# Kernel tuning notes

Measured on AMD Instinct MI355X. Metric: run time of the kernel, lower is better.

## Reference

```python
import jax, jax.numpy as jnp
import numpy as np
from jax import lax

DILATIONS = (1, 3, 5)
EPS = 1e-5
B, T, C, S, K = 8, 4096, 512, 64, 3


def _adain(x, s, w, b):
    # instance norm over time (axis=1), per (batch, channel), no learned affine;
    # style-conditioned affine: (1+gamma)*xn + beta
    h = s @ w + b                              # (B, 2C)
    gamma, beta = jnp.split(h, 2, axis=-1)     # (B, C) each
    mu = jnp.mean(x, axis=1, keepdims=True)
    var = jnp.var(x, axis=1, keepdims=True)
    xn = (x - mu) * lax.rsqrt(var + EPS)
    return (1.0 + gamma[:, None, :]) * xn + beta[:, None, :]


def _snake(x, alpha):
    # snake activation: x + (1/a) * sin(a*x)^2
    return x + (1.0 / alpha) * jnp.sin(alpha * x) ** 2


def _wn_conv(x, v, g, b, dilation):
    # weight-normalized dilated 1d conv; v: (K, Cin, Cout), norm over (K, Cin)
    norm = jnp.sqrt(jnp.sum(v * v, axis=(0, 1), keepdims=True))
    w = g[None, None, :] * v / norm
    y = lax.conv_general_dilated(x, w, window_strides=(1,), padding='SAME',
                                 rhs_dilation=(dilation,),
                                 dimension_numbers=('NWC', 'WIO', 'NWC'))
    return y + b


def setup_inputs() -> dict:
    key = jax.random.key(0)
    ks = jax.random.split(key, 6)
    return {
        'x': jax.random.normal(ks[0], (B, T, C), dtype=jnp.float32),
        's': jax.random.normal(ks[1], (B, S), dtype=jnp.float32),
        'fc1_w': jax.random.normal(ks[2], (3, S, 2 * C), dtype=jnp.float32) * 0.02,
        'fc1_b': jnp.zeros((3, 2 * C), dtype=jnp.float32),
        'alpha1': jnp.ones((3, 1, 1, C), dtype=jnp.float32),
        'conv1_v': jax.random.normal(ks[3], (3, K, C, C), dtype=jnp.float32),
        'conv1_g': jnp.ones((3, C), dtype=jnp.float32),
        'conv1_b': jnp.zeros((3, C), dtype=jnp.float32),
        'fc2_w': jax.random.normal(ks[4], (3, S, 2 * C), dtype=jnp.float32) * 0.02,
        'fc2_b': jnp.zeros((3, 2 * C), dtype=jnp.float32),
        'alpha2': jnp.ones((3, 1, 1, C), dtype=jnp.float32),
        'conv2_v': jax.random.normal(ks[5], (3, K, C, C), dtype=jnp.float32),
        'conv2_g': jnp.ones((3, C), dtype=jnp.float32),
        'conv2_b': jnp.zeros((3, C), dtype=jnp.float32),
    }


def reference(x, s, fc1_w, fc1_b, alpha1, conv1_v, conv1_g, conv1_b,
              fc2_w, fc2_b, alpha2, conv2_v, conv2_g, conv2_b):
    for i, d in enumerate(DILATIONS):
        xt = _adain(x, s, fc1_w[i], fc1_b[i])
        xt = _snake(xt, alpha1[i])
        xt = _wn_conv(xt, conv1_v[i], conv1_g[i], conv1_b[i], d)
        xt = _adain(xt, s, fc2_w[i], fc2_b[i])
        xt = _snake(xt, alpha2[i])
        xt = _wn_conv(xt, conv2_v[i], conv2_g[i], conv2_b[i], 1)
        x = xt + x
    return x
```

## Files before the change

### kernel.cpp

```cpp
#include <hip/hip_runtime.h>
#include <hip/hip_bf16.h>

#define B_ 8
#define T_ 4096
#define C_ 512
#define S_ 64
#define KT 3
#define EPSC 1e-5f
#define PADB 5
#define RB 4128

typedef __attribute__((ext_vector_type(8))) short bf16x8;
typedef __attribute__((ext_vector_type(4))) float f32x4;
typedef __attribute__((address_space(3))) unsigned int lds_u32_t;
typedef const __attribute__((address_space(1))) unsigned int glb_u32_t;

__device__ inline unsigned short f2bf(float x) {
    __hip_bfloat16 h = __float2bfloat16(x);
    return *reinterpret_cast<unsigned short*>(&h);
}

__global__ void norm_partial(const float* __restrict__ v1, const float* __restrict__ v2,
                             float* __restrict__ normsq) {
    int j = blockIdx.y;
    int i = j >> 1;
    const float* v = ((j & 1) ? v2 : v1) + (size_t)i * KT * C_ * C_;
    int r0 = blockIdx.x * 16;
    int tid = threadIdx.x;
    float a0 = 0.f, a1 = 0.f;
    for (int r = 0; r < 16; ++r) {
        const float* row = v + (size_t)(r0 + r) * C_;
        float x = row[tid];
        float y = row[tid + 256];
        a0 += x * x; a1 += y * y;
    }
    atomicAdd(&normsq[j * C_ + tid], a0);
    atomicAdd(&normsq[j * C_ + tid + 256], a1);
}

__global__ void wt_kernel(const float* __restrict__ v1, const float* __restrict__ v2,
                          const float* __restrict__ g1, const float* __restrict__ g2,
                          const float* __restrict__ normsq, unsigned short* __restrict__ wT) {
    __shared__ float tile[64][65];
    int jk = blockIdx.y;
    int j = jk / 3, k = jk % 3;
    int i = j >> 1;
    const float* v = ((j & 1) ? v2 : v1) + ((size_t)i * KT + k) * C_ * C_;
    const float* g = ((j & 1) ? g2 : g1) + (size_t)i * C_;
    int tci = (blockIdx.x >> 3) * 64;
    int tco = (blockIdx.x & 7) * 64;
    int tid = threadIdx.x;
    int lr = tid >> 6, lc = tid & 63;
    for (int rr = 0; rr < 16; ++rr) {
        int ci = rr * 4 + lr;
        tile[ci][lc] = v[(size_t)(tci + ci) * C_ + tco + lc];
    }
    __syncthreads();
    for (int rr = 0; rr < 16; ++rr) {
        int co_l = rr * 4 + lr;
        int co = tco + co_l;
        float w = g[co] * rsqrtf(normsq[j * C_ + co]) * tile[lc][co_l];
        wT[((size_t)j * KT + k) * C_ * C_ + (size_t)co * C_ + tci + lc] = f2bf(w);
    }
}

__global__ void zero_pads(unsigned short* __restrict__ zp) {
    int q = blockIdx.x * 256 + threadIdx.x;
    int b = q >> 11, r = q & 2047;
    int row = r >> 6;
    int col = (r & 63) * 8;
    int prow = row < PADB ? row : row + T_;
    uint4 zz = make_uint4(0u, 0u, 0u, 0u);
    *(uint4*)(zp + ((size_t)b * RB + prow) * C_ + col) = zz;
}

__global__ void stats_partial(const float* __restrict__ u, float* __restrict__ ssum,
                              float* __restrict__ ssq) {
    int c = blockIdx.y * 256 + threadIdx.x;
    int b = blockIdx.z;
    int t0 = blockIdx.x * 64;
    const float* p = u + ((size_t)b * T_ + t0) * C_ + c;
    float s1 = 0.f, s2 = 0.f;
    for (int t = 0; t < 64; ++t) {
        float x = p[(size_t)t * C_];
        s1 += x; s2 += x * x;
    }
    atomicAdd(&ssum[b * C_ + c], s1);
    atomicAdd(&ssq[b * C_ + c], s2);
}

__global__ void adain_finalize(const float* __restrict__ ssum, const float* __restrict__ ssq,
                               const float* __restrict__ s, const float* __restrict__ fcw,
                               const float* __restrict__ fcb,
                               float* __restrict__ scale, float* __restrict__ shift) {
    int idx = blockIdx.x * 256 + threadIdx.x;
    int b = idx >> 9, c = idx & (C_ - 1);
    float mu = ssum[idx] * (1.f / T_);
    float var = ssq[idx] * (1.f / T_) - mu * mu;
    var = fmaxf(var, 0.f);
    float gamma = fcb[c], beta = fcb[C_ + c];
    const float* sp = s + b * S_;
    for (int p = 0; p < S_; ++p) {
        float sv = sp[p];
        gamma += sv * fcw[p * 2 * C_ + c];
        beta  += sv * fcw[p * 2 * C_ + C_ + c];
    }
    float sc = (1.f + gamma) * rsqrtf(var + EPSC);
    scale[idx] = sc;
    shift[idx] = beta - mu * sc;
}

__global__ void act_kernel(const float* __restrict__ u, const float* __restrict__ scale,
                           const float* __restrict__ shift, const float* __restrict__ alpha,
                           unsigned short* __restrict__ zp) {
    size_t idx4 = (size_t)blockIdx.x * 256 + threadIdx.x;
    size_t e0 = idx4 * 4;
    int c = (int)(e0 & (C_ - 1));
    int b = (int)(e0 >> 21);
    const float4 xv = *(const float4*)(u + e0);
    const float4 scv = *(const float4*)(scale + b * C_ + c);
    const float4 shv = *(const float4*)(shift + b * C_ + c);
    const float4 av = *(const float4*)(alpha + c);
    float xx[4] = {xv.x, xv.y, xv.z, xv.w};
    float ss[4] = {scv.x, scv.y, scv.z, scv.w};
    float hh[4] = {shv.x, shv.y, shv.z, shv.w};
    float aa[4] = {av.x, av.y, av.z, av.w};
    ushort4 o;
    unsigned short r[4];
    #pragma unroll
    for (int q = 0; q < 4; ++q) {
        float val = xx[q] * ss[q] + hh[q];
        float sn = sinf(aa[q] * val);
        r[q] = f2bf(val + sn * sn / aa[q]);
    }
    o.x = r[0]; o.y = r[1]; o.z = r[2]; o.w = r[3];
    size_t dst = ((size_t)b * RB + PADB) * C_ + (e0 & (((size_t)1 << 21) - 1));
    *(ushort4*)(zp + dst) = o;
}

#define BM 128
#define BN 128
#define AR 160

__global__ __launch_bounds__(256) void conv_kernel(
    const unsigned short* __restrict__ zp, const unsigned short* __restrict__ wT,
    const float* __restrict__ bias, const float* __restrict__ residual,
    float* __restrict__ out, float* __restrict__ ssum, float* __restrict__ ssq, int dil) {
    __shared__ unsigned short As[AR * 64];
    __shared__ unsigned short Bs[3 * BN * 64];
    int tid = threadIdx.x;
    int m0 = blockIdx.x * BM;
    int b = m0 >> 12;
    int t0 = m0 & (T_ - 1);
    int n0 = blockIdx.y * BN;
    int wv = tid >> 6;
    int l = tid & 63;
    int wm = (wv >> 1) * 64, wn = (wv & 1) * 64;
    int l16 = l & 15, lg = l >> 4;

    const unsigned short* aBase = zp + ((size_t)b * RB + t0) * C_;
    const unsigned short* bBase = wT + (size_t)n0 * C_;

    f32x4 acc[4][4];
    #pragma unroll
    for (int a = 0; a < 4; ++a)
        #pragma unroll
        for (int q = 0; q < 4; ++q) acc[a][q] = (f32x4){0.f, 0.f, 0.f, 0.f};

    for (int ci0 = 0; ci0 < C_; ci0 += 64) {
        #pragma unroll
        for (int it = 0; it < 5; ++it) {
            int chunk = it * 256 + tid;
            int row = chunk >> 3, c = chunk & 7;
            const unsigned short* src = aBase + (size_t)row * C_ + ci0 + ((c ^ (row & 7)) * 8);
            __builtin_amdgcn_global_load_lds((glb_u32_t*)src,
                (lds_u32_t*)&As[(it * 256 + wv * 64) * 8], 16, 0, 0);
        }
        #pragma unroll
        for (int it = 0; it < 12; ++it) {
            int chunk = it * 256 + tid;
            int row = chunk >> 3, c = chunk & 7;
            int k = row >> 7, co = row & 127;
            const unsigned short* src = bBase + ((size_t)k * C_ + co) * C_ + ci0 + ((c ^ (row & 7)) * 8);
            __builtin_amdgcn_global_load_lds((glb_u32_t*)src,
                (lds_u32_t*)&Bs[(it * 256 + wv * 64) * 8], 16, 0, 0);
        }
        __syncthreads();

        #pragma unroll
        for (int ks = 0; ks < 2; ++ks) {
            #pragma unroll
            for (int k = 0; k < 3; ++k) {
                int sh = (k - 1) * dil + PADB;
                bf16x8 afr[4], bfr[4];
                #pragma unroll
                for (int mf = 0; mf < 4; ++mf) {
                    int row = wm + mf * 16 + l16 + sh;
                    afr[mf] = *(const bf16x8*)(&As[row * 64 + (((ks * 4 + lg) ^ (row & 7)) * 8)]);
                }
                #pragma unroll
                for (int nf = 0; nf < 4; ++nf) {
                    int row = wn + nf * 16 + l16;
                    bfr[nf] = *(const bf16x8*)(&Bs[(k * BN + row) * 64 + (((ks * 4 + lg) ^ (row & 7)) * 8)]);
                }
                #pragma unroll
                for (int mf = 0; mf < 4; ++mf)
                    #pragma unroll
                    for (int nf = 0; nf < 4; ++nf)
                        acc[mf][nf] = __builtin_amdgcn_mfma_f32_16x16x32_bf16(
                            afr[mf], bfr[nf], acc[mf][nf], 0, 0, 0);
            }
        }
        __syncthreads();
    }

    #pragma unroll
    for (int nf = 0; nf < 4; ++nf) {
        int co = n0 + wn + nf * 16 + l16;
        float bv = bias[co];
        float s1 = 0.f, s2 = 0.f;
        #pragma unroll
        for (int mf = 0; mf < 4; ++mf) {
            #pragma unroll
            for (int r = 0; r < 4; ++r) {
                int t = t0 + wm + mf * 16 + lg * 4 + r;
                size_t idx = ((size_t)b * T_ + t) * C_ + co;
                float val = acc[mf][nf][r] + bv;
                if (residual) val += residual[idx];
                out[idx] = val;
                s1 += val; s2 += val * val;
            }
        }
        s1 += __shfl_xor(s1, 16); s1 += __shfl_xor(s1, 32);
        s2 += __shfl_xor(s2, 16); s2 += __shfl_xor(s2, 32);
        if (lg == 0) {
            atomicAdd(&ssum[b * C_ + co], s1);
            atomicAdd(&ssq[b * C_ + co], s2);
        }
    }
}

extern "C" void kernel_launch(void* const* d_in, const int* in_sizes, int n_in,
                              void* d_out, int out_size, void* d_ws, size_t ws_size,
                              hipStream_t stream) {
    const float* x       = (const float*)d_in[0];
    const float* s       = (const float*)d_in[1];
    const float* fc1_w   = (const float*)d_in[2];
    const float* fc1_b   = (const float*)d_in[3];
    const float* alpha1  = (const float*)d_in[4];
    const float* conv1_v = (const float*)d_in[5];
    const float* conv1_g = (const float*)d_in[6];
    const float* conv1_b = (const float*)d_in[7];
    const float* fc2_w   = (const float*)d_in[8];
    const float* fc2_b   = (const float*)d_in[9];
    const float* alpha2  = (const float*)d_in[10];
    const float* conv2_v = (const float*)d_in[11];
    const float* conv2_g = (const float*)d_in[12];
    const float* conv2_b = (const float*)d_in[13];
    float* outp = (float*)d_out;

    char* ws = (char*)d_ws;
    const size_t MC = (size_t)B_ * T_ * C_;
    const size_t ZSZ = (size_t)B_ * RB * C_ * 2;
    unsigned short* z  = (unsigned short*)ws;
    float* y1          = (float*)(ws + ZSZ);
    unsigned short* wT = (unsigned short*)(ws + ZSZ + MC * 4);
    float* accum       = (float*)(ws + ZSZ + MC * 4 + (size_t)6 * KT * C_ * C_ * 2);
    float* normsq = accum;
    float* stats  = accum + 6 * C_;
    float* scale  = stats + 7 * 2 * B_ * C_;
    float* shift  = scale + B_ * C_;

    hipMemsetAsync(accum, 0, (size_t)(6 * C_ + 7 * 2 * B_ * C_) * sizeof(float), stream);
    zero_pads<<<64, 256, 0, stream>>>(z);
    norm_partial<<<dim3(96, 6), 256, 0, stream>>>(conv1_v, conv2_v, normsq);
    wt_kernel<<<dim3(64, 18), 256, 0, stream>>>(conv1_v, conv2_v, conv1_g, conv2_g, normsq, wT);

    const int dils[3] = {1, 3, 5};
    const float* xin = x;
    const int BC = B_ * C_;
    stats_partial<<<dim3(64, 2, 8), 256, 0, stream>>>(x, stats, stats + BC);

    for (int i = 0; i < 3; ++i) {
        float* p_in  = stats + (size_t)(2 * i) * 2 * BC;
        float* p_mid = stats + (size_t)(2 * i + 1) * 2 * BC;
        float* p_out = stats + (size_t)(2 * i + 2) * 2 * BC;

        adain_finalize<<<16, 256, 0, stream>>>(p_in, p_in + BC, s,
                                               fc1_w + (size_t)i * S_ * 2 * C_,
                                               fc1_b + (size_t)i * 2 * C_, scale, shift);
        act_kernel<<<16384, 256, 0, stream>>>(xin, scale, shift, alpha1 + (size_t)i * C_, z);
        conv_kernel<<<dim3(256, 4), 256, 0, stream>>>(
            z, wT + (size_t)(i * 2) * KT * C_ * C_, conv1_b + (size_t)i * C_,
            nullptr, y1, p_mid, p_mid + BC, dils[i]);

        adain_finalize<<<16, 256, 0, stream>>>(p_mid, p_mid + BC, s,
                                               fc2_w + (size_t)i * S_ * 2 * C_,
                                               fc2_b + (size_t)i * 2 * C_, scale, shift);
        act_kernel<<<16384, 256, 0, stream>>>(y1, scale, shift, alpha2 + (size_t)i * C_, z);
        conv_kernel<<<dim3(256, 4), 256, 0, stream>>>(
            z, wT + (size_t)(i * 2 + 1) * KT * C_ * C_, conv2_b + (size_t)i * C_,
            xin, outp, p_out, p_out + BC, 1);
        xin = outp;
    }
}
```

Before: 769.5 us.

## Enlarge conv GEMM tiles to 256x256 and double-buffer per-tap LDS staging

The conv kernel now uses 256x256 output tiles with 512 threads (8 waves, each 128x64) instead of 128x128 with 256 threads. Weight loading is split per kernel tap into double-buffered LDS, so the next tap or next channel chunk is fetched while MFMAs run on the current one. s_setprio is raised around the MFMA block. This aims to hide global-load latency and raise arithmetic intensity. The cost is 256 blocks (about one wave on the GPU), more registers for 32 accumulators, and a barrier per tap.

After: 773.8 us. About the same (+0.6%).

```diff
diff --git a/kernel.cpp b/kernel.cpp
--- a/kernel.cpp
+++ b/kernel.cpp
@@ -138,80 +138,100 @@
     *(ushort4*)(zp + dst) = o;
 }
 
-#define BM 128
-#define BN 128
-#define AR 160
-
-__global__ __launch_bounds__(256) void conv_kernel(
-    const unsigned short* __restrict__ zp, const unsigned short* __restrict__ wT,
+#define BM 256
+#define BN 256
+#define AR 272
+
+__global__ __launch_bounds__(512, 2) void conv_kernel(
+    const unsigned short* __restrict__ zp, const unsigned short* __restrict__ wTj,
     const float* __restrict__ bias, const float* __restrict__ residual,
     float* __restrict__ out, float* __restrict__ ssum, float* __restrict__ ssq, int dil) {
-    __shared__ unsigned short As[AR * 64];
-    __shared__ unsigned short Bs[3 * BN * 64];
+    __shared__ __align__(16) unsigned short As[2][AR * 64];
+    __shared__ __align__(16) unsigned short Bs[2][BN * 64];
     int tid = threadIdx.x;
+    int wv = tid >> 6, l = tid & 63;
+    int l16 = l & 15, lg = l >> 4;
     int m0 = blockIdx.x * BM;
-    int b = m0 >> 12;
-    int t0 = m0 & (T_ - 1);
+    int b = m0 >> 12, t0 = m0 & (T_ - 1);
     int n0 = blockIdx.y * BN;
-    int wv = tid >> 6;
-    int l = tid & 63;
-    int wm = (wv >> 1) * 64, wn = (wv & 1) * 64;
-    int l16 = l & 15, lg = l >> 4;
-
+    int wm = (wv >> 2) * 128, wn = (wv & 3) * 64;
     const unsigned short* aBase = zp + ((size_t)b * RB + t0) * C_;
-    const unsigned short* bBase = wT + (size_t)n0 * C_;
-
-    f32x4 acc[4][4];
+
+    f32x4 acc[8][4];
     #pragma unroll
-    for (int a = 0; a < 4; ++a)
+    for (int a = 0; a < 8; ++a)
         #pragma unroll
         for (int q = 0; q < 4; ++q) acc[a][q] = (f32x4){0.f, 0.f, 0.f, 0.f};
 
-    for (int ci0 = 0; ci0 < C_; ci0 += 64) {
-        #pragma unroll
-        for (int it = 0; it < 5; ++it) {
-            int chunk = it * 256 + tid;
+    auto STAGE_A = [&](int ci0, int pa) {
+        #pragma unroll
+        for (int it = 0; it < 4; ++it) {
+            int chunk = it * 512 + tid;
             int row = chunk >> 3, c = chunk & 7;
             const unsigned short* src = aBase + (size_t)row * C_ + ci0 + ((c ^ (row & 7)) * 8);
             __builtin_amdgcn_global_load_lds((glb_u32_t*)src,
-                (lds_u32_t*)&As[(it * 256 + wv * 64) * 8], 16, 0, 0);
-        }
-        #pragma unroll
-        for (int it = 0; it < 12; ++it) {
-            int chunk = it * 256 + tid;
+                (lds_u32_t*)&As[pa][(it * 512 + wv * 64) * 8], 16, 0, 0);
+        }
+        if (wv < 2) {
+            int chunk = 2048 + wv * 64 + l;
             int row = chunk >> 3, c = chunk & 7;
-            int k = row >> 7, co = row & 127;
-            const unsigned short* src = bBase + ((size_t)k * C_ + co) * C_ + ci0 + ((c ^ (row & 7)) * 8);
+            const unsigned short* src = aBase + (size_t)row * C_ + ci0 + ((c ^ (row & 7)) * 8);
             __builtin_amdgcn_global_load_lds((glb_u32_t*)src,
-                (lds_u32_t*)&Bs[(it * 256 + wv * 64) * 8], 16, 0, 0);
-        }
-        __syncthreads();
-
-        #pragma unroll
-        for (int ks = 0; ks < 2; ++ks) {
+                (lds_u32_t*)&As[pa][(2048 + wv * 64) * 8], 16, 0, 0);
+        }
+    };
+    auto STAGE_B = [&](int ci0, int k, int pb) {
+        #pragma unroll
+        for (int it = 0; it < 4; ++it) {
+            int chunk = it * 512 + tid;
+            int row = chunk >> 3, c = chunk & 7;
+            const unsigned short* src = wTj + ((size_t)k * C_ + n0 + row) * C_ + ci0 + ((c ^ (row & 7)) * 8);
+            __builtin_amdgcn_global_load_lds((glb_u32_t*)src,
+                (lds_u32_t*)&Bs[pb][(it * 512 + wv * 64) * 8], 16, 0, 0);
+        }
+    };
+
+    int pa = 0, pb = 0;
+    STAGE_A(0, 0);
+    STAGE_B(0, 0, 0);
+    __syncthreads();
+
+    for (int ci0 = 0; ci0 < C_; ci0 += 64) {
+        #pragma unroll
+        for (int k = 0; k < 3; ++k) {
+            if (k < 2) {
+                STAGE_B(ci0, k + 1, pb ^ 1);
+            } else if (ci0 < C_ - 64) {
+                STAGE_B(ci0 + 64, 0, pb ^ 1);
+                STAGE_A(ci0 + 64, pa ^ 1);
+            }
+            int sh = (k - 1) * dil + PADB;
+            __builtin_amdgcn_s_setprio(1);
             #pragma unroll
-            for (int k = 0; k < 3; ++k) {
-                int sh = (k - 1) * dil + PADB;
-                bf16x8 afr[4], bfr[4];
-                #pragma unroll
-                for (int mf = 0; mf < 4; ++mf) {
-                    int row = wm + mf * 16 + l16 + sh;
-                    afr[mf] = *(const bf16x8*)(&As[row * 64 + (((ks * 4 + lg) ^ (row & 7)) * 8)]);
-                }
+            for (int ks = 0; ks < 2; ++ks) {
+                bf16x8 afr[8], bfr[4];
                 #pragma unroll
                 for (int nf = 0; nf < 4; ++nf) {
                     int row = wn + nf * 16 + l16;
-                    bfr[nf] = *(const bf16x8*)(&Bs[(k * BN + row) * 64 + (((ks * 4 + lg) ^ (row & 7)) * 8)]);
+                    bfr[nf] = *(const bf16x8*)(&Bs[pb][row * 64 + (((ks * 4 + lg) ^ (row & 7)) * 8)]);
                 }
                 #pragma unroll
-                for (int mf = 0; mf < 4; ++mf)
+                for (int mf = 0; mf < 8; ++mf) {
+                    int row = wm + mf * 16 + l16 + sh;
+                    afr[mf] = *(const bf16x8*)(&As[pa][row * 64 + (((ks * 4 + lg) ^ (row & 7)) * 8)]);
+                }
+                #pragma unroll
+                for (int mf = 0; mf < 8; ++mf)
                     #pragma unroll
                     for (int nf = 0; nf < 4; ++nf)
                         acc[mf][nf] = __builtin_amdgcn_mfma_f32_16x16x32_bf16(
                             afr[mf], bfr[nf], acc[mf][nf], 0, 0, 0);
             }
-        }
-        __syncthreads();
+            __builtin_amdgcn_s_setprio(0);
+            __syncthreads();
+            pb ^= 1;
+            if (k == 2) pa ^= 1;
+        }
     }
 
     #pragma unroll
@@ -220,7 +240,7 @@
         float bv = bias[co];
         float s1 = 0.f, s2 = 0.f;
         #pragma unroll
-        for (int mf = 0; mf < 4; ++mf) {
+        for (int mf = 0; mf < 8; ++mf) {
             #pragma unroll
             for (int r = 0; r < 4; ++r) {
                 int t = t0 + wm + mf * 16 + lg * 4 + r;
@@ -290,7 +310,7 @@
                                                fc1_w + (size_t)i * S_ * 2 * C_,
                                                fc1_b + (size_t)i * 2 * C_, scale, shift);
         act_kernel<<<16384, 256, 0, stream>>>(xin, scale, shift, alpha1 + (size_t)i * C_, z);
-        conv_kernel<<<dim3(256, 4), 256, 0, stream>>>(
+        conv_kernel<<<dim3(128, 2), 512, 0, stream>>>(
             z, wT + (size_t)(i * 2) * KT * C_ * C_, conv1_b + (size_t)i * C_,
             nullptr, y1, p_mid, p_mid + BC, dils[i]);
 
@@ -298,7 +318,7 @@
                                                fc2_w + (size_t)i * S_ * 2 * C_,
                                                fc2_b + (size_t)i * 2 * C_, scale, shift);
         act_kernel<<<16384, 256, 0, stream>>>(y1, scale, shift, alpha2 + (size_t)i * C_, z);
-        conv_kernel<<<dim3(256, 4), 256, 0, stream>>>(
+        conv_kernel<<<dim3(128, 2), 512, 0, stream>>>(
             z, wT + (size_t)(i * 2 + 1) * KT * C_ * C_, conv2_b + (size_t)i * C_,
             xin, outp, p_out, p_out + BC, 1);
         xin = outp;
```
